# Kernel tuning notes

Measured on AMD Instinct MI355X. Metric: run time of the kernel, lower is better.

The kernel has to match this reference:

```python
import jax, jax.numpy as jnp
import numpy as np

N_USER = 100000
N_ITEM = 100000
E = 1000000
D_IN = 64
D_OUT = 64


def setup_inputs() -> dict:
    key = jax.random.key(0)
    ks = jax.random.split(key, 10)
    scale = 1.0 / np.sqrt(D_IN)
    return {
        "feat_user": jax.random.normal(ks[0], (N_USER, D_IN), jnp.float32),
        "feat_item": jax.random.normal(ks[1], (N_ITEM, D_IN), jnp.float32),
        "src_clicks": jax.random.randint(ks[2], (E,), 0, N_USER),        # user ids
        "dst_clicks": jax.random.randint(ks[3], (E,), 0, N_ITEM),        # item ids
        "src_clicked_by": jax.random.randint(ks[4], (E,), 0, N_ITEM),    # item ids
        "dst_clicked_by": jax.random.randint(ks[5], (E,), 0, N_USER),    # user ids
        "W_clicks": jax.random.normal(ks[6], (D_OUT, D_IN), jnp.float32) * scale,
        "b_clicks": jax.random.normal(ks[7], (D_OUT,), jnp.float32) * scale,
        "W_clicked_by": jax.random.normal(ks[8], (D_OUT, D_IN), jnp.float32) * scale,
        "b_clicked_by": jax.random.normal(ks[9], (D_OUT,), jnp.float32) * scale,
    }


def _relation_mean(feat_src, W, b, src, dst, n_dst):
    # per-relation Linear on src features (nn.Linear: x @ W.T + b)
    Wh = feat_src @ W.T + b                                  # [N_src, D_OUT]
    # copy_u + mean: gather messages along edges, segment-mean at dst
    msum = jax.ops.segment_sum(Wh[src], dst, num_segments=n_dst)   # [n_dst, D_OUT]
    deg = jax.ops.segment_sum(jnp.ones(src.shape[0], jnp.float32), dst,
                              num_segments=n_dst)                   # [n_dst]
    return msum / jnp.maximum(deg, 1.0)[:, None]             # zero-degree dsts -> 0


def reference(feat_user, feat_item, src_clicks, dst_clicks,
              src_clicked_by, dst_clicked_by,
              W_clicks, b_clicks, W_clicked_by, b_clicked_by):
    # relation (user, clicks, item): messages land on item nodes
    h_item = _relation_mean(feat_user, W_clicks, b_clicks,
                            src_clicks, dst_clicks, N_ITEM)
    # relation (item, clicked_by, user): messages land on user nodes
    h_user = _relation_mean(feat_item, W_clicked_by, b_clicked_by,
                            src_clicked_by, dst_clicked_by, N_USER)
    # cross-relation 'sum' reducer: each ntype receives from exactly one relation here
    return (h_user, h_item)
```

## Files before the change

### kernel.cpp

```cpp
#include <hip/hip_runtime.h>

#define D 64
#define BSH 7
#define BK 128
#define NBK 1024
#define CAP 2048
#define CHUNK 2048
#define EPT (CHUNK / 256)
#define TILE 64

static __device__ __forceinline__ unsigned short f2bf(float x) {
    unsigned int u = __float_as_uint(x);
    unsigned int r = (u + 0x7FFFu + ((u >> 16) & 1u)) >> 16;
    return (unsigned short)r;
}

__global__ __launch_bounds__(256) void phase1(
    const float* __restrict__ feat_u, const float* __restrict__ feat_i,
    const float* __restrict__ W_c, const float* __restrict__ b_c,
    const float* __restrict__ W_cb, const float* __restrict__ b_cb,
    unsigned short* __restrict__ Whb_u, unsigned short* __restrict__ Whb_i,
    const int* __restrict__ srcA, const int* __restrict__ dstA,
    const int* __restrict__ srcB, const int* __restrict__ dstB,
    int* __restrict__ bcur,
    unsigned int* __restrict__ ebufA, unsigned int* __restrict__ ebufB,
    int n_user, int n_item, int n_edges, int ntile, int eb) {
    __shared__ union {
        struct { float FT[D * TILE]; float WT[D * TILE]; } lin;
        struct { int hist[NBK], obase[NBK], cur[NBK], ps[256];
                 unsigned int stage[CHUNK]; unsigned short sbkt[CHUNK]; } fil;
    } sh;
    int t = threadIdx.x;
    int blk = blockIdx.x;

    if (blk < 2 * ntile) {
        int rel = (blk >= ntile);
        int tile = rel ? blk - ntile : blk;
        const float* feat = rel ? feat_i : feat_u;
        const float* W    = rel ? W_cb   : W_c;
        const float* bia  = rel ? b_cb   : b_c;
        unsigned short* out = rel ? Whb_i : Whb_u;
        int n = rel ? n_item : n_user;
        int row0 = tile * TILE;
        if (row0 >= n) return;
        int lr = t >> 4;
        int k4 = (t & 15) * 4;
        #pragma unroll
        for (int it = 0; it < 4; ++it) {
            int r = lr + it * 16;
            int grow = row0 + r; if (grow > n - 1) grow = n - 1;
            float4 f = *(const float4*)(feat + (size_t)grow * D + k4);
            sh.lin.FT[(k4 + 0) * TILE + r] = f.x;
            sh.lin.FT[(k4 + 1) * TILE + r] = f.y;
            sh.lin.FT[(k4 + 2) * TILE + r] = f.z;
            sh.lin.FT[(k4 + 3) * TILE + r] = f.w;
            float4 w = *(const float4*)(W + r * D + k4);
            sh.lin.WT[(k4 + 0) * TILE + r] = w.x;
            sh.lin.WT[(k4 + 1) * TILE + r] = w.y;
            sh.lin.WT[(k4 + 2) * TILE + r] = w.z;
            sh.lin.WT[(k4 + 3) * TILE + r] = w.w;
        }
        __syncthreads();
        int c0 = (t & 15) * 4;
        int r0 = (t >> 4) * 4;
        float4 bv = *(const float4*)(bia + c0);
        float acc[4][4];
        #pragma unroll
        for (int ri = 0; ri < 4; ++ri) {
            acc[ri][0] = bv.x; acc[ri][1] = bv.y; acc[ri][2] = bv.z; acc[ri][3] = bv.w;
        }
        #pragma unroll 8
        for (int k = 0; k < D; ++k) {
            float4 w = *(const float4*)(sh.lin.WT + k * TILE + c0);
            float4 f = *(const float4*)(sh.lin.FT + k * TILE + r0);
            acc[0][0] = fmaf(f.x, w.x, acc[0][0]); acc[0][1] = fmaf(f.x, w.y, acc[0][1]);
            acc[0][2] = fmaf(f.x, w.z, acc[0][2]); acc[0][3] = fmaf(f.x, w.w, acc[0][3]);
            acc[1][0] = fmaf(f.y, w.x, acc[1][0]); acc[1][1] = fmaf(f.y, w.y, acc[1][1]);
            acc[1][2] = fmaf(f.y, w.z, acc[1][2]); acc[1][3] = fmaf(f.y, w.w, acc[1][3]);
            acc[2][0] = fmaf(f.z, w.x, acc[2][0]); acc[2][1] = fmaf(f.z, w.y, acc[2][1]);
            acc[2][2] = fmaf(f.z, w.z, acc[2][2]); acc[2][3] = fmaf(f.z, w.w, acc[2][3]);
            acc[3][0] = fmaf(f.w, w.x, acc[3][0]); acc[3][1] = fmaf(f.w, w.y, acc[3][1]);
            acc[3][2] = fmaf(f.w, w.z, acc[3][2]); acc[3][3] = fmaf(f.w, w.w, acc[3][3]);
        }
        #pragma unroll
        for (int ri = 0; ri < 4; ++ri) {
            int row = row0 + r0 + ri;
            if (row < n) {
                ushort4 o;
                o.x = f2bf(acc[ri][0]); o.y = f2bf(acc[ri][1]);
                o.z = f2bf(acc[ri][2]); o.w = f2bf(acc[ri][3]);
                *(ushort4*)(out + (size_t)row * D + c0) = o;
            }
        }
    } else {
        int fb = blk - 2 * ntile;
        int rel = (fb >= eb);
        int chunk = rel ? fb - eb : fb;
        const int* src = rel ? srcB : srcA;
        const int* dst = rel ? dstB : dstA;
        int* bu = bcur + rel * NBK;
        unsigned int* ebuf = rel ? ebufB : ebufA;
        for (int i = t; i < NBK; i += 256) sh.fil.hist[i] = 0;
        __syncthreads();
        int base = chunk * CHUNK;
        int m = n_edges - base; if (m > CHUNK) m = CHUNK;
        unsigned int packed[EPT];
        int bk[EPT];
        if (m == CHUNK) {
            const int4* s4p = (const int4*)(src + base);
            const int4* d4p = (const int4*)(dst + base);
            #pragma unroll
            for (int q = 0; q < EPT / 4; ++q) {
                int4 s = s4p[t * (EPT / 4) + q];
                int4 dd = d4p[t * (EPT / 4) + q];
                int sv[4] = {s.x, s.y, s.z, s.w};
                int dv[4] = {dd.x, dd.y, dd.z, dd.w};
                #pragma unroll
                for (int jj = 0; jj < 4; ++jj) {
                    int j = q * 4 + jj;
                    bk[j] = ((unsigned)dv[jj]) >> BSH;
                    packed[j] = (unsigned int)sv[jj] | (((unsigned int)dv[jj] & (BK - 1)) << 24);
                    atomicAdd(&sh.fil.hist[bk[j]], 1);
                }
            }
        } else {
            #pragma unroll
            for (int j = 0; j < EPT; ++j) {
                int e = base + t * EPT + j;
                if (e < n_edges) {
                    int d = dst[e];
                    int s = src[e];
                    bk[j] = ((unsigned)d) >> BSH;
                    packed[j] = (unsigned int)s | (((unsigned int)d & (BK - 1)) << 24);
                    atomicAdd(&sh.fil.hist[bk[j]], 1);
                } else bk[j] = -1;
            }
        }
        __syncthreads();
        int a[4]; int s4 = 0;
        #pragma unroll
        for (int j = 0; j < 4; ++j) { a[j] = sh.fil.hist[4 * t + j]; s4 += a[j]; }
        sh.fil.ps[t] = s4;
        __syncthreads();
        for (int o = 1; o < 256; o <<= 1) {
            int x = (t >= o) ? sh.fil.ps[t - o] : 0;
            __syncthreads();
            sh.fil.ps[t] += x;
            __syncthreads();
        }
        int ex = sh.fil.ps[t] - s4;
        #pragma unroll
        for (int j = 0; j < 4; ++j) {
            sh.fil.obase[4 * t + j] = ex;
            sh.fil.cur[4 * t + j] = ex;
            ex += a[j];
        }
        __syncthreads();
        for (int b = t; b < NBK; b += 256) {
            int c = sh.fil.hist[b];
            if (c) sh.fil.obase[b] = b * CAP + atomicAdd(&bu[b], c) - sh.fil.obase[b];
        }
        #pragma unroll
        for (int j = 0; j < EPT; ++j) {
            if (bk[j] >= 0) {
                int p = atomicAdd(&sh.fil.cur[bk[j]], 1);
                sh.fil.stage[p] = packed[j];
                sh.fil.sbkt[p] = (unsigned short)bk[j];
            }
        }
        __syncthreads();
        for (int i = t; i < m; i += 256) {
            int b = sh.fil.sbkt[i];
            int pos = sh.fil.obase[b] + i;
            if ((unsigned)(pos - b * CAP) < CAP)
                ebuf[pos] = sh.fil.stage[i];
        }
    }
}

__global__ __launch_bounds__(256) void bucket_gather(
    const unsigned short* __restrict__ Whb_u, const unsigned short* __restrict__ Whb_i,
    const unsigned int* __restrict__ ebufA, const unsigned int* __restrict__ ebufB,
    const int* __restrict__ bcur,
    float* __restrict__ h_user, float* __restrict__ h_item,
    int n_user, int n_item) {
    int rel = blockIdx.y;
    const unsigned short* Wh = rel ? Whb_u : Whb_i;
    const unsigned int* ebuf = rel ? ebufB : ebufA;
    float* out = rel ? h_item : h_user;
    int n = rel ? n_item : n_user;
    int b = blockIdx.x;
    int cnt = bcur[rel * NBK + b]; if (cnt > CAP) cnt = CAP;
    size_t base = (size_t)b * CAP;
    __shared__ unsigned int ssrc[CAP];
    __shared__ int hist[BK], ofs[BK], cur[BK];
    int t = threadIdx.x;
    if (t < BK) hist[t] = 0;
    __syncthreads();
    unsigned int pk[CAP / 256];
    #pragma unroll
    for (int j = 0; j < CAP / 256; ++j) {
        int i = t + j * 256;
        if (i < cnt) {
            pk[j] = ebuf[base + i];
            atomicAdd(&hist[pk[j] >> 24], 1);
        }
    }
    __syncthreads();
    if (t < BK) ofs[t] = hist[t];
    __syncthreads();
    for (int o = 1; o < BK; o <<= 1) {
        int x = (t >= o && t < BK) ? ofs[t - o] : 0;
        __syncthreads();
        if (t < BK) ofs[t] += x;
        __syncthreads();
    }
    if (t < BK) { int ex = ofs[t] - hist[t]; ofs[t] = ex; cur[t] = ex; }
    __syncthreads();
    #pragma unroll
    for (int j = 0; j < CAP / 256; ++j) {
        int i = t + j * 256;
        if (i < cnt) {
            int nd = pk[j] >> 24;
            int p = atomicAdd(&cur[nd], 1);
            ssrc[p] = pk[j] & 0xFFFFFFu;
        }
    }
    __syncthreads();
    int lane = t & 63;
    int w = t >> 6;
    int half = lane >> 5;
    int lp = lane & 31;
    int node0 = b * BK;
    for (int nd = w; nd < BK; nd += 4) {
        int node = node0 + nd;
        if (node >= n) break;
        int st = ofs[nd];
        int dg = hist[nd];
        int en = st + dg;
        float l[8], h[8];
        #pragma unroll
        for (int q = 0; q < 8; ++q) { l[q] = 0.f; h[q] = 0.f; }
        for (int j = st; j < en; j += 16) {
            unsigned int v[8];
            #pragma unroll
            for (int q = 0; q < 8; ++q) {
                int e = j + 2 * q + half;
                v[q] = 0;
                if (e < en) v[q] = ((const unsigned int*)(Wh + (size_t)ssrc[e] * D))[lp];
            }
            #pragma unroll
            for (int q = 0; q < 8; ++q) {
                l[q] += __uint_as_float(v[q] << 16);
                h[q] += __uint_as_float(v[q] & 0xFFFF0000u);
            }
        }
        float lo = ((l[0] + l[1]) + (l[2] + l[3])) + ((l[4] + l[5]) + (l[6] + l[7]));
        float hi = ((h[0] + h[1]) + (h[2] + h[3])) + ((h[4] + h[5]) + (h[6] + h[7]));
        lo += __shfl_xor(lo, 32, 64);
        hi += __shfl_xor(hi, 32, 64);
        if (half == 0) {
            float inv = 1.f / fmaxf((float)dg, 1.f);
            float2 o; o.x = lo * inv; o.y = hi * inv;
            *(float2*)(out + (size_t)node * D + 2 * lp) = o;
        }
    }
}

extern "C" void kernel_launch(void* const* d_in, const int* in_sizes, int n_in,
                              void* d_out, int out_size, void* d_ws, size_t ws_size,
                              hipStream_t stream) {
    const float* feat_user      = (const float*)d_in[0];
    const float* feat_item      = (const float*)d_in[1];
    const int*   src_clicks     = (const int*)d_in[2];
    const int*   dst_clicks     = (const int*)d_in[3];
    const int*   src_clicked_by = (const int*)d_in[4];
    const int*   dst_clicked_by = (const int*)d_in[5];
    const float* W_clicks       = (const float*)d_in[6];
    const float* b_clicks       = (const float*)d_in[7];
    const float* W_clicked_by   = (const float*)d_in[8];
    const float* b_clicked_by   = (const float*)d_in[9];

    const int n_user  = in_sizes[0] / D;
    const int n_item  = in_sizes[1] / D;
    const int n_edges = in_sizes[2];

    float* out = (float*)d_out;
    float* h_user = out;
    float* h_item = out + (size_t)n_user * D;

    unsigned short* Whb_user = (unsigned short*)d_ws;
    unsigned short* Whb_item = Whb_user + (size_t)n_user * D;
    int* ip        = (int*)(Whb_item + (size_t)n_item * D);
    unsigned int* ebuf_user = (unsigned int*)ip;  ip += NBK * CAP;
    unsigned int* ebuf_item = (unsigned int*)ip;  ip += NBK * CAP;
    int* bcur = ip;

    hipMemsetAsync(bcur, 0, 2 * NBK * sizeof(int), stream);

    int ntile = (max(n_user, n_item) + TILE - 1) / TILE;
    int eb = (n_edges + CHUNK - 1) / CHUNK;
    phase1<<<2 * ntile + 2 * eb, 256, 0, stream>>>(
        feat_user, feat_item, W_clicks, b_clicks, W_clicked_by, b_clicked_by,
        Whb_user, Whb_item,
        src_clicked_by, dst_clicked_by, src_clicks, dst_clicks,
        bcur, ebuf_user, ebuf_item,
        n_user, n_item, n_edges, ntile, eb);

    int nbkt = (max(n_user, n_item) + BK - 1) / BK;
    bucket_gather<<<dim3(nbkt, 2), 256, 0, stream>>>(
        Whb_user, Whb_item, ebuf_user, ebuf_item, bcur,
        h_user, h_item, n_user, n_item);
}
```

Baseline: 242.1 us.

## Scatter edges directly to buckets, swizzle linear LDS, wave-scan bucket offsets

The edge-binning path drops the block-wide prefix scan and shared staging buffer. Each edge now claims its slot with a shared atomic on a per-bucket cursor seeded from the global atomic, and is written straight to global memory. CHUNK doubles so each block handles more edges, and index loads are issued before the histogram is cleared. The linear tile gets an XOR swizzle on its LDS layout to cut bank conflicts, and the gather kernel replaces its barrier-heavy scan with a wavefront shuffle scan. The cost is less coalesced, non-ordered global stores for edges and more registers per thread.

```diff
diff --git a/kernel.cpp b/kernel.cpp
--- a/kernel.cpp
+++ b/kernel.cpp
@@ -5,7 +5,7 @@
 #define BK 128
 #define NBK 1024
 #define CAP 2048
-#define CHUNK 2048
+#define CHUNK 4096
 #define EPT (CHUNK / 256)
 #define TILE 64
 
@@ -27,8 +27,7 @@
     int n_user, int n_item, int n_edges, int ntile, int eb) {
     __shared__ union {
         struct { float FT[D * TILE]; float WT[D * TILE]; } lin;
-        struct { int hist[NBK], obase[NBK], cur[NBK], ps[256];
-                 unsigned int stage[CHUNK]; unsigned short sbkt[CHUNK]; } fil;
+        struct { int hist[NBK], cur[NBK]; } fil;
     } sh;
     int t = threadIdx.x;
     int blk = blockIdx.x;
@@ -44,25 +43,29 @@
         int row0 = tile * TILE;
         if (row0 >= n) return;
         int lr = t >> 4;
-        int k4 = (t & 15) * 4;
+        int kq = t & 15;
+        int k4 = kq * 4;
         #pragma unroll
         for (int it = 0; it < 4; ++it) {
             int r = lr + it * 16;
             int grow = row0 + r; if (grow > n - 1) grow = n - 1;
             float4 f = *(const float4*)(feat + (size_t)grow * D + k4);
-            sh.lin.FT[(k4 + 0) * TILE + r] = f.x;
-            sh.lin.FT[(k4 + 1) * TILE + r] = f.y;
-            sh.lin.FT[(k4 + 2) * TILE + r] = f.z;
-            sh.lin.FT[(k4 + 3) * TILE + r] = f.w;
+            int sw = (((r >> 2) ^ kq) & 15) * 4 + (r & 3);
+            sh.lin.FT[(k4 + 0) * TILE + sw] = f.x;
+            sh.lin.FT[(k4 + 1) * TILE + sw] = f.y;
+            sh.lin.FT[(k4 + 2) * TILE + sw] = f.z;
+            sh.lin.FT[(k4 + 3) * TILE + sw] = f.w;
             float4 w = *(const float4*)(W + r * D + k4);
-            sh.lin.WT[(k4 + 0) * TILE + r] = w.x;
-            sh.lin.WT[(k4 + 1) * TILE + r] = w.y;
-            sh.lin.WT[(k4 + 2) * TILE + r] = w.z;
-            sh.lin.WT[(k4 + 3) * TILE + r] = w.w;
+            sh.lin.WT[(k4 + 0) * TILE + sw] = w.x;
+            sh.lin.WT[(k4 + 1) * TILE + sw] = w.y;
+            sh.lin.WT[(k4 + 2) * TILE + sw] = w.z;
+            sh.lin.WT[(k4 + 3) * TILE + sw] = w.w;
         }
         __syncthreads();
-        int c0 = (t & 15) * 4;
-        int r0 = (t >> 4) * 4;
+        int cbW = t & 15;
+        int cbF = t >> 4;
+        int c0 = cbW * 4;
+        int r0 = cbF * 4;
         float4 bv = *(const float4*)(bia + c0);
         float acc[4][4];
         #pragma unroll
@@ -71,8 +74,9 @@
         }
         #pragma unroll 8
         for (int k = 0; k < D; ++k) {
-            float4 w = *(const float4*)(sh.lin.WT + k * TILE + c0);
-            float4 f = *(const float4*)(sh.lin.FT + k * TILE + r0);
+            int kq2 = k >> 2;
+            float4 w = *(const float4*)(sh.lin.WT + k * TILE + (((cbW ^ kq2) & 15) << 2));
+            float4 f = *(const float4*)(sh.lin.FT + k * TILE + (((cbF ^ kq2) & 15) << 2));
             acc[0][0] = fmaf(f.x, w.x, acc[0][0]); acc[0][1] = fmaf(f.x, w.y, acc[0][1]);
             acc[0][2] = fmaf(f.x, w.z, acc[0][2]); acc[0][3] = fmaf(f.x, w.w, acc[0][3]);
             acc[1][0] = fmaf(f.y, w.x, acc[1][0]); acc[1][1] = fmaf(f.y, w.y, acc[1][1]);
@@ -100,8 +104,6 @@
         const int* dst = rel ? dstB : dstA;
         int* bu = bcur + rel * NBK;
         unsigned int* ebuf = rel ? ebufB : ebufA;
-        for (int i = t; i < NBK; i += 256) sh.fil.hist[i] = 0;
-        __syncthreads();
         int base = chunk * CHUNK;
         int m = n_edges - base; if (m > CHUNK) m = CHUNK;
         unsigned int packed[EPT];
@@ -109,21 +111,29 @@
         if (m == CHUNK) {
             const int4* s4p = (const int4*)(src + base);
             const int4* d4p = (const int4*)(dst + base);
+            int4 sv[EPT / 4], dv[EPT / 4];
             #pragma unroll
             for (int q = 0; q < EPT / 4; ++q) {
-                int4 s = s4p[t * (EPT / 4) + q];
-                int4 dd = d4p[t * (EPT / 4) + q];
-                int sv[4] = {s.x, s.y, s.z, s.w};
-                int dv[4] = {dd.x, dd.y, dd.z, dd.w};
+                sv[q] = s4p[t * (EPT / 4) + q];
+                dv[q] = d4p[t * (EPT / 4) + q];
+            }
+            for (int i = t; i < NBK; i += 256) sh.fil.hist[i] = 0;
+            __syncthreads();
+            #pragma unroll
+            for (int q = 0; q < EPT / 4; ++q) {
+                int s4a[4] = {sv[q].x, sv[q].y, sv[q].z, sv[q].w};
+                int d4a[4] = {dv[q].x, dv[q].y, dv[q].z, dv[q].w};
                 #pragma unroll
                 for (int jj = 0; jj < 4; ++jj) {
                     int j = q * 4 + jj;
-                    bk[j] = ((unsigned)dv[jj]) >> BSH;
-                    packed[j] = (unsigned int)sv[jj] | (((unsigned int)dv[jj] & (BK - 1)) << 24);
+                    bk[j] = ((unsigned)d4a[jj]) >> BSH;
+                    packed[j] = (unsigned int)s4a[jj] | (((unsigned int)d4a[jj] & (BK - 1)) << 24);
                     atomicAdd(&sh.fil.hist[bk[j]], 1);
                 }
             }
         } else {
+            for (int i = t; i < NBK; i += 256) sh.fil.hist[i] = 0;
+            __syncthreads();
             #pragma unroll
             for (int j = 0; j < EPT; ++j) {
                 int e = base + t * EPT + j;
@@ -137,43 +147,18 @@
             }
         }
         __syncthreads();
-        int a[4]; int s4 = 0;
-        #pragma unroll
-        for (int j = 0; j < 4; ++j) { a[j] = sh.fil.hist[4 * t + j]; s4 += a[j]; }
-        sh.fil.ps[t] = s4;
+        for (int b2 = t; b2 < NBK; b2 += 256) {
+            int c = sh.fil.hist[b2];
+            if (c) sh.fil.cur[b2] = b2 * CAP + atomicAdd(&bu[b2], c);
+        }
         __syncthreads();
-        for (int o = 1; o < 256; o <<= 1) {
-            int x = (t >= o) ? sh.fil.ps[t - o] : 0;
-            __syncthreads();
-            sh.fil.ps[t] += x;
-            __syncthreads();
-        }
-        int ex = sh.fil.ps[t] - s4;
-        #pragma unroll
-        for (int j = 0; j < 4; ++j) {
-            sh.fil.obase[4 * t + j] = ex;
-            sh.fil.cur[4 * t + j] = ex;
-            ex += a[j];
-        }
-        __syncthreads();
-        for (int b = t; b < NBK; b += 256) {
-            int c = sh.fil.hist[b];
-            if (c) sh.fil.obase[b] = b * CAP + atomicAdd(&bu[b], c) - sh.fil.obase[b];
-        }
         #pragma unroll
         for (int j = 0; j < EPT; ++j) {
             if (bk[j] >= 0) {
-                int p = atomicAdd(&sh.fil.cur[bk[j]], 1);
-                sh.fil.stage[p] = packed[j];
-                sh.fil.sbkt[p] = (unsigned short)bk[j];
-            }
-        }
-        __syncthreads();
-        for (int i = t; i < m; i += 256) {
-            int b = sh.fil.sbkt[i];
-            int pos = sh.fil.obase[b] + i;
-            if ((unsigned)(pos - b * CAP) < CAP)
-                ebuf[pos] = sh.fil.stage[i];
+                int pos = atomicAdd(&sh.fil.cur[bk[j]], 1);
+                if ((unsigned)(pos - bk[j] * CAP) < CAP)
+                    ebuf[pos] = packed[j];
+            }
         }
     }
 }
@@ -194,6 +179,7 @@
     size_t base = (size_t)b * CAP;
     __shared__ unsigned int ssrc[CAP];
     __shared__ int hist[BK], ofs[BK], cur[BK];
+    __shared__ int w0tot;
     int t = threadIdx.x;
     if (t < BK) hist[t] = 0;
     __syncthreads();
@@ -207,15 +193,20 @@
         }
     }
     __syncthreads();
-    if (t < BK) ofs[t] = hist[t];
-    __syncthreads();
-    for (int o = 1; o < BK; o <<= 1) {
-        int x = (t >= o && t < BK) ? ofs[t - o] : 0;
+    {
+        int lane = t & 63;
+        int v = (t < BK) ? hist[t] : 0;
+        int inc = v;
+        #pragma unroll
+        for (int o = 1; o < 64; o <<= 1) {
+            int x = __shfl_up(inc, o, 64);
+            if (lane >= o) inc += x;
+        }
+        if (t == 63) w0tot = inc;
         __syncthreads();
-        if (t < BK) ofs[t] += x;
-        __syncthreads();
-    }
-    if (t < BK) { int ex = ofs[t] - hist[t]; ofs[t] = ex; cur[t] = ex; }
+        if (t >= 64 && t < BK) inc += w0tot;
+        if (t < BK) { int ex = inc - v; ofs[t] = ex; cur[t] = ex; }
+    }
     __syncthreads();
     #pragma unroll
     for (int j = 0; j < CAP / 256; ++j) {
```

Measured after the change: 218.8 us. 1.11x faster.
